# Kernel optimization log

Hardware: AMD Instinct MI355X
Metric: run time of the kernel (lower is better)

## Reference

```python
import jax, jax.numpy as jnp
import numpy as np
from jax import lax

K = 8  # diffusion channels
T = 3  # diffusion steps


def setup_inputs() -> dict:
    key = jax.random.key(0)
    k1, k2, k3 = jax.random.split(key, 3)
    x = jax.random.normal(k1, (16, 1, 512, 512), dtype=jnp.float32)
    # per-step conv weights [T, out=k, in=1, kh, kw] and biases [T, k]
    W = jax.random.normal(k2, (T, K, 1, 3, 3), dtype=jnp.float32) * 0.1
    b = jax.random.normal(k3, (T, K), dtype=jnp.float32) * 0.1
    return {"x": x, "W": W, "b": b}


def _g(d):
    # mode 1 edge-stopping function: exp(-|d| / (1 + d^2))
    return jnp.exp(-jnp.abs(d) / (1.0 + d * d))


def reference(x, W, b):
    in_x = x  # [N,1,H,W]
    for t in range(T):
        d1 = lax.conv_general_dilated(
            in_x, W[t], window_strides=(1, 1), padding="SAME",
            dimension_numbers=("NCHW", "OIHW", "NCHW"),
        ) + b[t][None, :, None, None]  # [N,K,H,W]
        features = _g(d1) * d1
        # squash_tensor: sum over the K channels, keep channel dim of 1
        in_x = in_x - jnp.sum(features, axis=1, keepdims=True) / K
    return in_x
```

## Files before the change

### kernel.cpp

```cpp
#include <hip/hip_runtime.h>

static constexpr int IMG = 512;

__device__ __forceinline__ float gd_acc(float d, float acc) {
    const float t    = fmaf(d, d, 1.0f);
    const float rinv = __builtin_amdgcn_rcpf(t);
    const float e    = __builtin_amdgcn_exp2f(
                           -1.442695040888963f * __builtin_fabsf(d) * rinv);
    return fmaf(e, d, acc);
}

__global__ __launch_bounds__(256) void ad_step(
    const float* __restrict__ in, float* __restrict__ outp,
    const float* __restrict__ Wt, const float* __restrict__ bt)
{
    const int tid = threadIdx.x;
    const int x0  = blockIdx.x * 64 + (tid & 15) * 4;
    const int y   = blockIdx.y * 16 + (tid >> 4);
    const float* __restrict__ src = in + (size_t)blockIdx.z * (IMG * IMG);

    float L[3][12];
    const bool xfast = (x0 >= 4) && (x0 <= 504);
#pragma unroll
    for (int dy = 0; dy < 3; ++dy) {
        const int yy = y + dy - 1;
        const bool rowok = (unsigned)yy < (unsigned)IMG;
        if (xfast && rowok) {
            const float* p = src + yy * IMG + x0 - 4;
            *(float4*)&L[dy][0] = *(const float4*)(p);
            *(float4*)&L[dy][4] = *(const float4*)(p + 4);
            *(float4*)&L[dy][8] = *(const float4*)(p + 8);
        } else {
#pragma unroll
            for (int j = 0; j < 12; ++j) {
                const int col = x0 - 4 + j;
                L[dy][j] = (rowok && (unsigned)col < (unsigned)IMG)
                               ? src[yy * IMG + col] : 0.f;
            }
        }
    }

    float acc[4] = {0.f, 0.f, 0.f, 0.f};
#pragma unroll
    for (int k = 0; k < 8; ++k) {
        const float w0 = Wt[9*k+0], w1 = Wt[9*k+1], w2 = Wt[9*k+2];
        const float w3 = Wt[9*k+3], w4 = Wt[9*k+4], w5 = Wt[9*k+5];
        const float w6 = Wt[9*k+6], w7 = Wt[9*k+7], w8 = Wt[9*k+8];
        const float bk = bt[k];
#pragma unroll
        for (int i = 0; i < 4; ++i) {
            float d = bk;
            d = fmaf(w0, L[0][i+3], d);
            d = fmaf(w1, L[0][i+4], d);
            d = fmaf(w2, L[0][i+5], d);
            d = fmaf(w3, L[1][i+3], d);
            d = fmaf(w4, L[1][i+4], d);
            d = fmaf(w5, L[1][i+5], d);
            d = fmaf(w6, L[2][i+3], d);
            d = fmaf(w7, L[2][i+4], d);
            d = fmaf(w8, L[2][i+5], d);
            acc[i] = gd_acc(d, acc[i]);
        }
    }

    float4 v;
    v.x = L[1][4] - acc[0] * 0.125f;
    v.y = L[1][5] - acc[1] * 0.125f;
    v.z = L[1][6] - acc[2] * 0.125f;
    v.w = L[1][7] - acc[3] * 0.125f;
    *(float4*)&outp[(size_t)blockIdx.z * (IMG * IMG) + y * IMG + x0] = v;
}

static constexpr int TXF = 64;
static constexpr int TYF = 16;
static constexpr int LST = 72;
static constexpr int SROWS  = TYF + 6;
static constexpr int NSTAGE = SROWS * 18;

template<int WOFF, int NR, int RLO, int NG, bool TO_GLOBAL>
__device__ __forceinline__ void diffuse_step(
    const float* __restrict__ prev, float* __restrict__ cur,
    const float* __restrict__ Wt, const float* __restrict__ bt,
    int xoff, int ty0, int tx0, int tid, float* __restrict__ gout)
{
    constexpr int LOADW  = WOFF ? 8 : 6;
    constexpr int NITEMS = NR * NG;

    float L0[LOADW], L1[LOADW], L2[LOADW];
    {
        const int idx0 = (tid < NITEMS) ? tid : 0;
        const int rr = idx0 / NG, j = idx0 - rr * NG;
        const float* base = prev + (RLO + rr - 1) * LST + 4 * j;
        *(float4*)&L0[0] = *(const float4*)(base);
        *(float4*)&L1[0] = *(const float4*)(base + LST);
        *(float4*)&L2[0] = *(const float4*)(base + 2 * LST);
        if (WOFF) {
            *(float4*)&L0[4] = *(const float4*)(base + 4);
            *(float4*)&L1[4] = *(const float4*)(base + LST + 4);
            *(float4*)&L2[4] = *(const float4*)(base + 2 * LST + 4);
        } else {
            *(float2*)&L0[4] = *(const float2*)(base + 4);
            *(float2*)&L1[4] = *(const float2*)(base + LST + 4);
            *(float2*)&L2[4] = *(const float2*)(base + 2 * LST + 4);
        }
    }

    for (int idx = tid; idx < NITEMS; idx += 64) {
        float P0[LOADW], P1[LOADW], P2[LOADW];
        {
            const int nidx = (idx + 64 < NITEMS) ? (idx + 64) : idx;
            const int rr = nidx / NG, j = nidx - rr * NG;
            const float* base = prev + (RLO + rr - 1) * LST + 4 * j;
            *(float4*)&P0[0] = *(const float4*)(base);
            *(float4*)&P1[0] = *(const float4*)(base + LST);
            *(float4*)&P2[0] = *(const float4*)(base + 2 * LST);
            if (WOFF) {
                *(float4*)&P0[4] = *(const float4*)(base + 4);
                *(float4*)&P1[4] = *(const float4*)(base + LST + 4);
                *(float4*)&P2[4] = *(const float4*)(base + 2 * LST + 4);
            } else {
                *(float2*)&P0[4] = *(const float2*)(base + 4);
                *(float2*)&P1[4] = *(const float2*)(base + LST + 4);
                *(float2*)&P2[4] = *(const float2*)(base + 2 * LST + 4);
            }
        }

        const int rr = idx / NG, j = idx - rr * NG;
        const int r  = RLO + rr, c0 = 4 * j;

        float acc[4] = {0.f, 0.f, 0.f, 0.f};
#pragma unroll
        for (int k = 0; k < 8; ++k) {
            const float w0 = Wt[9*k+0], w1 = Wt[9*k+1], w2 = Wt[9*k+2];
            const float w3 = Wt[9*k+3], w4 = Wt[9*k+4], w5 = Wt[9*k+5];
            const float w6 = Wt[9*k+6], w7 = Wt[9*k+7], w8 = Wt[9*k+8];
            const float bk = bt[k];
#pragma unroll
            for (int i = 0; i < 4; ++i) {
                float d = bk;
                d = fmaf(w0, L0[WOFF+i],   d);
                d = fmaf(w1, L0[WOFF+i+1], d);
                d = fmaf(w2, L0[WOFF+i+2], d);
                d = fmaf(w3, L1[WOFF+i],   d);
                d = fmaf(w4, L1[WOFF+i+1], d);
                d = fmaf(w5, L1[WOFF+i+2], d);
                d = fmaf(w6, L2[WOFF+i],   d);
                d = fmaf(w7, L2[WOFF+i+1], d);
                d = fmaf(w8, L2[WOFF+i+2], d);
                acc[i] = gd_acc(d, acc[i]);
            }
        }

        float4 v;
        v.x = L1[WOFF+1] - acc[0] * 0.125f;
        v.y = L1[WOFF+2] - acc[1] * 0.125f;
        v.z = L1[WOFF+3] - acc[2] * 0.125f;
        v.w = L1[WOFF+4] - acc[3] * 0.125f;

        const int gy = ty0 - 3 + r;
        if (TO_GLOBAL) {
            *(float4*)&gout[gy * IMG + tx0 + c0] = v;
        } else {
            const bool ry  = (unsigned)gy < (unsigned)IMG;
            const int  gx0 = xoff + c0;
            v.x = (ry && (unsigned)(gx0 + 0) < (unsigned)IMG) ? v.x : 0.f;
            v.y = (ry && (unsigned)(gx0 + 1) < (unsigned)IMG) ? v.y : 0.f;
            v.z = (ry && (unsigned)(gx0 + 2) < (unsigned)IMG) ? v.z : 0.f;
            v.w = (ry && (unsigned)(gx0 + 3) < (unsigned)IMG) ? v.w : 0.f;
            *(float4*)&cur[r * LST + c0] = v;
        }

#pragma unroll
        for (int q = 0; q < LOADW; ++q) { L0[q] = P0[q]; L1[q] = P1[q]; L2[q] = P2[q]; }
    }
}

__global__ __launch_bounds__(64) void deep_ad_fused(
    const float* __restrict__ x, const float* __restrict__ W,
    const float* __restrict__ b, float* __restrict__ out)
{
    __shared__ float A[SROWS * LST];
    __shared__ float Bs[SROWS * LST];

    const int tid = threadIdx.x;
    const int tx0 = blockIdx.x * TXF;
    const int ty0 = blockIdx.y * TYF;
    const float* xin  = x   + (size_t)blockIdx.z * (IMG * IMG);
    float*       gout = out + (size_t)blockIdx.z * (IMG * IMG);

    {
        float4 sv[7];
#pragma unroll
        for (int q = 0; q < 7; ++q) {
            const int item = tid + 64 * q;
            const int rr = item / 18, j = item - rr * 18;
            const int gy = ty0 - 3 + rr;
            const int gx = tx0 - 4 + 4 * j;
            float4 v = {0.f, 0.f, 0.f, 0.f};
            if (item < NSTAGE && (unsigned)gy < (unsigned)IMG && (unsigned)gx < (unsigned)IMG)
                v = *(const float4*)(xin + gy * IMG + gx);
            sv[q] = v;
        }
#pragma unroll
        for (int q = 0; q < 7; ++q) {
            const int item = tid + 64 * q;
            if (item < NSTAGE) *(float4*)&A[item * 4] = sv[q];
        }
    }
    __syncthreads();

    diffuse_step<1, TYF + 4, 1, 17, false>(A,  Bs, W + 0,   b + 0,  tx0 - 2, ty0, tx0, tid, nullptr);
    __syncthreads();
    diffuse_step<0, TYF + 2, 2, 17, false>(Bs, A,  W + 72,  b + 8,  tx0 - 1, ty0, tx0, tid, nullptr);
    __syncthreads();
    diffuse_step<0, TYF,     3, 16, true >(A, nullptr, W + 144, b + 16, 0, ty0, tx0, tid, gout);
}

extern "C" void kernel_launch(void* const* d_in, const int* in_sizes, int n_in,
                              void* d_out, int out_size, void* d_ws, size_t ws_size,
                              hipStream_t stream)
{
    const float* x = (const float*)d_in[0];
    const float* W = (const float*)d_in[1];
    const float* b = (const float*)d_in[2];
    float* out = (float*)d_out;
    const int N = in_sizes[0] / (IMG * IMG);

    const size_t imgBytes = (size_t)N * IMG * IMG * sizeof(float);
    if (ws_size >= imgBytes) {
        float* ws = (float*)d_ws;
        dim3 g(IMG / 64, IMG / 16, N);
        ad_step<<<g, 256, 0, stream>>>(x,   out, W + 0,   b + 0);
        ad_step<<<g, 256, 0, stream>>>(out, ws,  W + 72,  b + 8);
        ad_step<<<g, 256, 0, stream>>>(ws,  out, W + 144, b + 16);
    } else {
        dim3 grid(IMG / TXF, IMG / TYF, N);
        deep_ad_fused<<<grid, 64, 0, stream>>>(x, W, b, out);
    }
}
```

Before: 115.4 us.

## Always use fused three-step shared-memory kernel with 256-thread 64x32 tiles

Removes the three-kernel path that round-trips each diffusion step through global memory. The fused tiled kernel now always runs, with the tile enlarged to 64x32 and the block to 256 threads. The manual software prefetch in the step loop is removed, and each thread loads its own rows directly. The change cuts global traffic and launch count, in exchange for redundant halo computation and higher shared-memory use per block.

```diff
diff --git a/kernel.cpp b/kernel.cpp
--- a/kernel.cpp
+++ b/kernel.cpp
@@ -1,6 +1,11 @@
 #include <hip/hip_runtime.h>
 
 static constexpr int IMG = 512;
+static constexpr int TX  = 64;
+static constexpr int TY  = 32;
+static constexpr int LST = 72;
+static constexpr int SROWS  = TY + 6;
+static constexpr int NSTAGE = SROWS * (LST / 4);
 
 __device__ __forceinline__ float gd_acc(float d, float acc) {
     const float t    = fmaf(d, d, 1.0f);
@@ -10,87 +15,19 @@
     return fmaf(e, d, acc);
 }
 
-__global__ __launch_bounds__(256) void ad_step(
-    const float* __restrict__ in, float* __restrict__ outp,
-    const float* __restrict__ Wt, const float* __restrict__ bt)
-{
-    const int tid = threadIdx.x;
-    const int x0  = blockIdx.x * 64 + (tid & 15) * 4;
-    const int y   = blockIdx.y * 16 + (tid >> 4);
-    const float* __restrict__ src = in + (size_t)blockIdx.z * (IMG * IMG);
-
-    float L[3][12];
-    const bool xfast = (x0 >= 4) && (x0 <= 504);
-#pragma unroll
-    for (int dy = 0; dy < 3; ++dy) {
-        const int yy = y + dy - 1;
-        const bool rowok = (unsigned)yy < (unsigned)IMG;
-        if (xfast && rowok) {
-            const float* p = src + yy * IMG + x0 - 4;
-            *(float4*)&L[dy][0] = *(const float4*)(p);
-            *(float4*)&L[dy][4] = *(const float4*)(p + 4);
-            *(float4*)&L[dy][8] = *(const float4*)(p + 8);
-        } else {
-#pragma unroll
-            for (int j = 0; j < 12; ++j) {
-                const int col = x0 - 4 + j;
-                L[dy][j] = (rowok && (unsigned)col < (unsigned)IMG)
-                               ? src[yy * IMG + col] : 0.f;
-            }
-        }
-    }
-
-    float acc[4] = {0.f, 0.f, 0.f, 0.f};
-#pragma unroll
-    for (int k = 0; k < 8; ++k) {
-        const float w0 = Wt[9*k+0], w1 = Wt[9*k+1], w2 = Wt[9*k+2];
-        const float w3 = Wt[9*k+3], w4 = Wt[9*k+4], w5 = Wt[9*k+5];
-        const float w6 = Wt[9*k+6], w7 = Wt[9*k+7], w8 = Wt[9*k+8];
-        const float bk = bt[k];
-#pragma unroll
-        for (int i = 0; i < 4; ++i) {
-            float d = bk;
-            d = fmaf(w0, L[0][i+3], d);
-            d = fmaf(w1, L[0][i+4], d);
-            d = fmaf(w2, L[0][i+5], d);
-            d = fmaf(w3, L[1][i+3], d);
-            d = fmaf(w4, L[1][i+4], d);
-            d = fmaf(w5, L[1][i+5], d);
-            d = fmaf(w6, L[2][i+3], d);
-            d = fmaf(w7, L[2][i+4], d);
-            d = fmaf(w8, L[2][i+5], d);
-            acc[i] = gd_acc(d, acc[i]);
-        }
-    }
-
-    float4 v;
-    v.x = L[1][4] - acc[0] * 0.125f;
-    v.y = L[1][5] - acc[1] * 0.125f;
-    v.z = L[1][6] - acc[2] * 0.125f;
-    v.w = L[1][7] - acc[3] * 0.125f;
-    *(float4*)&outp[(size_t)blockIdx.z * (IMG * IMG) + y * IMG + x0] = v;
-}
-
-static constexpr int TXF = 64;
-static constexpr int TYF = 16;
-static constexpr int LST = 72;
-static constexpr int SROWS  = TYF + 6;
-static constexpr int NSTAGE = SROWS * 18;
-
 template<int WOFF, int NR, int RLO, int NG, bool TO_GLOBAL>
 __device__ __forceinline__ void diffuse_step(
     const float* __restrict__ prev, float* __restrict__ cur,
     const float* __restrict__ Wt, const float* __restrict__ bt,
     int xoff, int ty0, int tx0, int tid, float* __restrict__ gout)
 {
-    constexpr int LOADW  = WOFF ? 8 : 6;
     constexpr int NITEMS = NR * NG;
+    for (int idx = tid; idx < NITEMS; idx += 256) {
+        const int rr = idx / NG, j = idx - rr * NG;
+        const int r  = RLO + rr, c0 = 4 * j;
+        const float* base = prev + (r - 1) * LST + c0;
 
-    float L0[LOADW], L1[LOADW], L2[LOADW];
-    {
-        const int idx0 = (tid < NITEMS) ? tid : 0;
-        const int rr = idx0 / NG, j = idx0 - rr * NG;
-        const float* base = prev + (RLO + rr - 1) * LST + 4 * j;
+        float L0[8], L1[8], L2[8];
         *(float4*)&L0[0] = *(const float4*)(base);
         *(float4*)&L1[0] = *(const float4*)(base + LST);
         *(float4*)&L2[0] = *(const float4*)(base + 2 * LST);
@@ -103,30 +40,6 @@
             *(float2*)&L1[4] = *(const float2*)(base + LST + 4);
             *(float2*)&L2[4] = *(const float2*)(base + 2 * LST + 4);
         }
-    }
-
-    for (int idx = tid; idx < NITEMS; idx += 64) {
-        float P0[LOADW], P1[LOADW], P2[LOADW];
-        {
-            const int nidx = (idx + 64 < NITEMS) ? (idx + 64) : idx;
-            const int rr = nidx / NG, j = nidx - rr * NG;
-            const float* base = prev + (RLO + rr - 1) * LST + 4 * j;
-            *(float4*)&P0[0] = *(const float4*)(base);
-            *(float4*)&P1[0] = *(const float4*)(base + LST);
-            *(float4*)&P2[0] = *(const float4*)(base + 2 * LST);
-            if (WOFF) {
-                *(float4*)&P0[4] = *(const float4*)(base + 4);
-                *(float4*)&P1[4] = *(const float4*)(base + LST + 4);
-                *(float4*)&P2[4] = *(const float4*)(base + 2 * LST + 4);
-            } else {
-                *(float2*)&P0[4] = *(const float2*)(base + 4);
-                *(float2*)&P1[4] = *(const float2*)(base + LST + 4);
-                *(float2*)&P2[4] = *(const float2*)(base + 2 * LST + 4);
-            }
-        }
-
-        const int rr = idx / NG, j = idx - rr * NG;
-        const int r  = RLO + rr, c0 = 4 * j;
 
         float acc[4] = {0.f, 0.f, 0.f, 0.f};
 #pragma unroll
@@ -169,51 +82,50 @@
             v.w = (ry && (unsigned)(gx0 + 3) < (unsigned)IMG) ? v.w : 0.f;
             *(float4*)&cur[r * LST + c0] = v;
         }
-
-#pragma unroll
-        for (int q = 0; q < LOADW; ++q) { L0[q] = P0[q]; L1[q] = P1[q]; L2[q] = P2[q]; }
     }
 }
 
-__global__ __launch_bounds__(64) void deep_ad_fused(
+__global__ __launch_bounds__(256) void deep_ad_fused256(
     const float* __restrict__ x, const float* __restrict__ W,
     const float* __restrict__ b, float* __restrict__ out)
 {
-    __shared__ float A[SROWS * LST];
+    __shared__ float A [SROWS * LST];
     __shared__ float Bs[SROWS * LST];
 
     const int tid = threadIdx.x;
-    const int tx0 = blockIdx.x * TXF;
-    const int ty0 = blockIdx.y * TYF;
+    const int tx0 = blockIdx.x * TX;
+    const int ty0 = blockIdx.y * TY;
     const float* xin  = x   + (size_t)blockIdx.z * (IMG * IMG);
     float*       gout = out + (size_t)blockIdx.z * (IMG * IMG);
 
     {
-        float4 sv[7];
+        float4 sv[3];
 #pragma unroll
-        for (int q = 0; q < 7; ++q) {
-            const int item = tid + 64 * q;
-            const int rr = item / 18, j = item - rr * 18;
-            const int gy = ty0 - 3 + rr;
-            const int gx = tx0 - 4 + 4 * j;
+        for (int q = 0; q < 3; ++q) {
+            const int item = tid + 256 * q;
             float4 v = {0.f, 0.f, 0.f, 0.f};
-            if (item < NSTAGE && (unsigned)gy < (unsigned)IMG && (unsigned)gx < (unsigned)IMG)
-                v = *(const float4*)(xin + gy * IMG + gx);
+            if (item < NSTAGE) {
+                const int rr = item / 18, j = item - rr * 18;
+                const int gy = ty0 - 3 + rr;
+                const int gx = tx0 - 4 + 4 * j;
+                if ((unsigned)gy < (unsigned)IMG && (unsigned)gx < (unsigned)IMG)
+                    v = *(const float4*)(xin + gy * IMG + gx);
+            }
             sv[q] = v;
         }
 #pragma unroll
-        for (int q = 0; q < 7; ++q) {
-            const int item = tid + 64 * q;
+        for (int q = 0; q < 3; ++q) {
+            const int item = tid + 256 * q;
             if (item < NSTAGE) *(float4*)&A[item * 4] = sv[q];
         }
     }
     __syncthreads();
 
-    diffuse_step<1, TYF + 4, 1, 17, false>(A,  Bs, W + 0,   b + 0,  tx0 - 2, ty0, tx0, tid, nullptr);
+    diffuse_step<1, TY + 4, 1, 17, false>(A,  Bs, W,       b,      tx0 - 2, ty0, tx0, tid, nullptr);
     __syncthreads();
-    diffuse_step<0, TYF + 2, 2, 17, false>(Bs, A,  W + 72,  b + 8,  tx0 - 1, ty0, tx0, tid, nullptr);
+    diffuse_step<0, TY + 2, 2, 17, false>(Bs, A,  W + 72,  b + 8,  tx0 - 1, ty0, tx0, tid, nullptr);
     __syncthreads();
-    diffuse_step<0, TYF,     3, 16, true >(A, nullptr, W + 144, b + 16, 0, ty0, tx0, tid, gout);
+    diffuse_step<0, TY,     3, 16, true >(A, nullptr, W + 144, b + 16, 0, ty0, tx0, tid, gout);
 }
 
 extern "C" void kernel_launch(void* const* d_in, const int* in_sizes, int n_in,
@@ -226,15 +138,6 @@
     float* out = (float*)d_out;
     const int N = in_sizes[0] / (IMG * IMG);
 
-    const size_t imgBytes = (size_t)N * IMG * IMG * sizeof(float);
-    if (ws_size >= imgBytes) {
-        float* ws = (float*)d_ws;
-        dim3 g(IMG / 64, IMG / 16, N);
-        ad_step<<<g, 256, 0, stream>>>(x,   out, W + 0,   b + 0);
-        ad_step<<<g, 256, 0, stream>>>(out, ws,  W + 72,  b + 8);
-        ad_step<<<g, 256, 0, stream>>>(ws,  out, W + 144, b + 16);
-    } else {
-        dim3 grid(IMG / TXF, IMG / TYF, N);
-        deep_ad_fused<<<grid, 64, 0, stream>>>(x, W, b, out);
-    }
+    dim3 grid(IMG / TX, IMG / TY, N);
+    deep_ad_fused256<<<grid, 256, 0, stream>>>(x, W, b, out);
 }
```

Result: slower. 135.2 us (+17.2%).
